# Kernel optimization log

Measured on AMD Instinct MI355X. Metric: run time of the kernel, lower is better.

## Reference

```python
import jax, jax.numpy as jnp
import numpy as np


def setup_inputs() -> dict:
    key = jax.random.key(0)
    ks = jax.random.split(key, 7)
    B, S, D, F, E = 4, 2048, 1024, 4096, 8
    scale = 0.02
    return {
        "x": jax.random.normal(ks[0], (B, S, D), dtype=jnp.float32),
        "gate_w": jax.random.normal(ks[1], (D, E), dtype=jnp.float32) * scale,
        "gate_b": jnp.zeros((E,), dtype=jnp.float32),
        "w1": jax.random.normal(ks[2], (E, D, F), dtype=jnp.float32) * scale,
        "b1": jnp.zeros((E, F), dtype=jnp.float32),
        "w2": jax.random.normal(ks[3], (E, F, D), dtype=jnp.float32) * scale,
        "b2": jnp.zeros((E, D), dtype=jnp.float32),
        "top_k": 2,
    }


def reference(x, gate_w, gate_b, w1, b1, w2, b2, top_k):
    B, S, D = x.shape
    E = w1.shape[0]
    xf = x.reshape(-1, D)                      # [T, D], T = B*S
    T = xf.shape[0]

    # Router: top-k logits, softmax over the selected k (as in torch code)
    logits = xf @ gate_w + gate_b              # [T, E]
    rw, sel = jax.lax.top_k(logits, top_k)     # [T, k], [T, k]
    w = jax.nn.softmax(rw, axis=-1)            # [T, k]

    # Dense combine weights: combine[t, e] = sum_k w[t,k] * (sel[t,k]==e)
    combine = jnp.zeros((T, E), dtype=xf.dtype)
    combine = combine.at[jnp.arange(T)[:, None], sel].add(w)

    # Loop over small fixed expert count; each expert FFN on all tokens,
    # weighted by combine (zero for unrouted tokens). Dropout p honored as 0 (eval).
    out = jnp.zeros_like(xf)
    for e in range(E):
        h = jax.nn.gelu(xf @ w1[e] + b1[e], approximate=False)  # torch F.gelu = exact
        out = out + combine[:, e:e + 1] * (h @ w2[e] + b2[e])
    return out.reshape(B, S, D)
```

## Files before the change

kernel.cpp:

```cpp
#include <hip/hip_runtime.h>
#include <math.h>

#define T_TOK 8192
#define DDIM  1024
#define FDIM  4096
#define NEXP  8
#define MAXT  136
#define NSLOT (2 * T_TOK)

typedef __attribute__((ext_vector_type(8))) short short8;
typedef __attribute__((ext_vector_type(4))) float f32x4;
typedef unsigned short u16;
typedef unsigned int   u32;

typedef const __attribute__((address_space(1))) u32* gp_t;
typedef       __attribute__((address_space(3))) u32* lp_t;

__device__ __forceinline__ void gload16(const void* g, void* l) {
  __builtin_amdgcn_global_load_lds((gp_t)g, (lp_t)l, 16, 0, 0);
}

#define VM6 asm volatile("s_waitcnt vmcnt(6)" ::: "memory")
#define VM0 asm volatile("s_waitcnt vmcnt(0)" ::: "memory")
#define SBAR __builtin_amdgcn_s_barrier()
#define SCHED0 __builtin_amdgcn_sched_barrier(0)

__device__ __forceinline__ u16 f2bf(float f) {
  u32 u = __float_as_uint(f);
  u = u + 0x7FFFu + ((u >> 16) & 1u);
  return (u16)(u >> 16);
}

__device__ __forceinline__ int imin(int a, int b) { return a < b ? a : b; }

__device__ __forceinline__ float gelu_fast(float v) {
  float u = 0.7978845608f * (v + 0.044715f * v * v * v);
  float t2 = __expf(2.f * u);
  float th = 1.f - 2.f / (t2 + 1.f);
  return 0.5f * v * (1.f + th);
}

__device__ __forceinline__ int xcd_swz(int orig, int nwg) {
  int xcd = orig & 7;
  int q = nwg >> 3, r = nwg & 7;
  int base = (xcd < r) ? xcd * (q + 1) : r * (q + 1) + (xcd - r) * q;
  return base + (orig >> 3);
}

__global__ __launch_bounds__(256) void router_kernel(
    const float* __restrict__ x, const float* __restrict__ gw,
    const float* __restrict__ gb, u16* __restrict__ xb,
    int* __restrict__ counts, int* __restrict__ sel, float* __restrict__ wts)
{
  const int t    = blockIdx.x * 4 + (threadIdx.x >> 6);
  const int lane = threadIdx.x & 63;
  const float* xr = x + (size_t)t * DDIM;
  u16* xbr = xb + (size_t)t * DDIM;
  float lg[NEXP];
  #pragma unroll
  for (int e = 0; e < NEXP; e++) lg[e] = 0.f;
  #pragma unroll
  for (int i = 0; i < 4; i++) {
    int d0 = i * 256 + lane * 4;
    float4 v = *(const float4*)(xr + d0);
    ushort4 o;
    o.x = f2bf(v.x); o.y = f2bf(v.y); o.z = f2bf(v.z); o.w = f2bf(v.w);
    *(ushort4*)(xbr + d0) = o;
    const float* g = gw + (size_t)d0 * NEXP;
    #pragma unroll
    for (int e = 0; e < NEXP; e++)
      lg[e] += v.x * g[e] + v.y * g[NEXP + e] + v.z * g[2 * NEXP + e] + v.w * g[3 * NEXP + e];
  }
  #pragma unroll
  for (int off = 32; off > 0; off >>= 1) {
    #pragma unroll
    for (int e = 0; e < NEXP; e++) lg[e] += __shfl_down(lg[e], off);
  }
  if (lane == 0) {
    float v0 = -1e30f, v1 = -1e30f; int s0 = 0, s1 = 0;
    #pragma unroll
    for (int e = 0; e < NEXP; e++) {
      float v = lg[e] + gb[e];
      if (v > v0) { v1 = v0; s1 = s0; v0 = v; s0 = e; }
      else if (v > v1) { v1 = v; s1 = e; }
    }
    float a  = expf(v1 - v0);
    float w0 = 1.f / (1.f + a);
    sel[t * 2] = s0; sel[t * 2 + 1] = s1;
    wts[t * 2] = w0; wts[t * 2 + 1] = 1.f - w0;
    atomicAdd(&counts[s0], 1); atomicAdd(&counts[s1], 1);
  }
}

__global__ __launch_bounds__(256) void scan_assign_kernel(
    const int* __restrict__ counts, const int* __restrict__ sel,
    const float* __restrict__ wts,
    int* __restrict__ offsets, int* __restrict__ map_e, int* __restrict__ map_r,
    int* __restrict__ nT, int* __restrict__ stok, float* __restrict__ swgt)
{
  __shared__ int spos[NEXP];
  if (threadIdx.x == 0) {
    int run = 0, nt = 0;
    for (int e = 0; e < NEXP; e++) {
      offsets[e] = run; spos[e] = run;
      int c = counts[e];
      int ntile = (c + 127) >> 7;
      for (int i = 0; i < ntile; i++) { map_e[nt] = e; map_r[nt] = i * 128; nt++; }
      run += c;
    }
    nT[0] = nt;
  }
  __syncthreads();
  for (int t = threadIdx.x; t < T_TOK; t += 256) {
    #pragma unroll
    for (int k = 0; k < 2; k++) {
      int e = sel[t * 2 + k];
      int p = atomicAdd(&spos[e], 1);
      stok[p] = t; swgt[p] = wts[t * 2 + k];
    }
  }
}

__global__ __launch_bounds__(256) void xgather_kernel(
    const u16* __restrict__ xb, const int* __restrict__ stok,
    u16* __restrict__ Xg)
{
  const int s = blockIdx.x * 2 + (threadIdx.x >> 7);
  const int u = threadIdx.x & 127;
  int tok = stok[s]; if ((u32)tok >= T_TOK) tok = 0;
  const uint4* src = (const uint4*)(xb + (size_t)tok * DDIM);
  uint4* dst = (uint4*)(Xg + (size_t)s * DDIM);
  dst[u] = src[u];
}

__global__ __launch_bounds__(256) void wtrans_kernel(
    const float* __restrict__ in, u16* __restrict__ out, int M, int N)
{
  const int e = blockIdx.z;
  in  += (size_t)e * M * N;
  out += (size_t)e * M * N;
  const int r0 = blockIdx.y * 128;
  const int c0 = blockIdx.x * 64;
  __shared__ float tile[128][65];
  const int tid = threadIdx.x;
  const int lr = tid >> 4;
  const int lc = (tid & 15) * 4;
  #pragma unroll
  for (int p = 0; p < 8; p++) {
    int r = p * 16 + lr;
    float4 v = *(const float4*)(in + (size_t)(r0 + r) * N + (c0 + lc));
    tile[r][lc] = v.x; tile[r][lc + 1] = v.y; tile[r][lc + 2] = v.z; tile[r][lc + 3] = v.w;
  }
  __syncthreads();
  const int oc = tid >> 4;
  const int om = (tid & 15) * 8;
  #pragma unroll
  for (int p = 0; p < 4; p++) {
    int c = p * 16 + oc;
    short8 o;
    #pragma unroll
    for (int j = 0; j < 8; j++) o[j] = (short)f2bf(tile[om + j][c]);
    *(short8*)(out + (size_t)(c0 + c) * M + (r0 + om)) = o;
  }
}

__global__ __launch_bounds__(512, 2) void gemm1_kernel(
    const u16* __restrict__ Xg, const u16* __restrict__ W1T,
    const float* __restrict__ B1,
    const int* __restrict__ counts, const int* __restrict__ offsets,
    const int* __restrict__ map_e, const int* __restrict__ map_r,
    const int* __restrict__ nT, u16* __restrict__ H)
{
  __shared__ __align__(16) char lds[3 * 49152];
  const int gid   = xcd_swz(blockIdx.x, gridDim.x);
  const int n_idx = gid / MAXT;
  const int t_idx = gid - n_idx * MAXT;
  if (t_idx >= nT[0]) return;
  const int e    = map_e[t_idx];
  const int row0 = map_r[t_idx];
  const int cnt  = counts[e];
  const int off  = offsets[e];
  const int n0   = n_idx * 256;

  const int tid = threadIdx.x, wave = tid >> 6, lane = tid & 63;
  const int lr = lane & 15, lq = lane >> 4;
  const int wr = wave >> 2, wc = wave & 3;
  const int l3 = lane >> 3;
  const int usrc = (lane & 7) ^ l3;

  const char* gA[2]; const char* gB[4];
  #pragma unroll
  for (int i = 0; i < 2; i++) {
    int rA = imin(off + row0 + wave * 16 + i * 8 + l3, NSLOT - 1);
    gA[i] = (const char*)Xg + (size_t)rA * 2048 + usrc * 16;
  }
  #pragma unroll
  for (int i = 0; i < 4; i++) {
    int rB = e * FDIM + n0 + wave * 32 + i * 8 + l3;
    gB[i] = (const char*)W1T + (size_t)rB * 2048 + usrc * 16;
  }

  auto stage = [&](int slot, int kByte) {
    char* base = lds + slot * 49152;
    #pragma unroll
    for (int i = 0; i < 2; i++)
      gload16(gA[i] + kByte, base + wave * 2048 + i * 1024 + lane * 16);
    #pragma unroll
    for (int i = 0; i < 4; i++)
      gload16(gB[i] + kByte, base + 16384 + wave * 4096 + i * 1024 + lane * 16);
  };

  f32x4 acc[4][4] = {};
  auto compute = [&](int slot) {
    const u16* A  = (const u16*)(lds + slot * 49152);
    const u16* Bp = (const u16*)(lds + slot * 49152 + 16384);
    #pragma unroll
    for (int ks = 0; ks < 2; ks++) {
      const int uu = ((ks * 4 + lq) ^ (lr & 7)) * 8;
      short8 a[4], b[4];
      #pragma unroll
      for (int n = 0; n < 4; n++)
        b[n] = *(const short8*)&Bp[(wc * 64 + n * 16 + lr) * 64 + uu];
      #pragma unroll
      for (int m = 0; m < 4; m++)
        a[m] = *(const short8*)&A[(wr * 64 + m * 16 + lr) * 64 + uu];
      #pragma unroll
      for (int m = 0; m < 4; m++)
        #pragma unroll
        for (int n = 0; n < 4; n++)
          acc[m][n] = __builtin_amdgcn_mfma_f32_16x16x32_bf16(a[m], b[n], acc[m][n], 0, 0, 0);
    }
  };

  stage(0, 0); stage(1, 128);
  VM6; SCHED0; SBAR; SCHED0;
  #pragma unroll 1
  for (int t = 0; t < 16; t++) {
    if (t + 2 < 16) stage((t + 2) % 3, (t + 2) * 128);
    compute(t % 3);
    SCHED0;
    if (t + 2 < 16)       { VM6; }
    else if (t + 2 == 16) { VM0; }
    SCHED0; SBAR; SCHED0;
  }

  #pragma unroll
  for (int m = 0; m < 4; m++) {
    int rloc = wr * 64 + m * 16 + lq * 4;
    #pragma unroll
    for (int j = 0; j < 4; j++) {
      int r = rloc + j;
      if (row0 + r < cnt) {
        u16* Hrow = H + (size_t)(off + row0 + r) * FDIM;
        #pragma unroll
        for (int n = 0; n < 4; n++) {
          int col = n0 + wc * 64 + n * 16 + lr;
          float v = acc[m][n][j] + B1[e * FDIM + col];
          Hrow[col] = f2bf(gelu_fast(v));
        }
      }
    }
  }
}

__global__ __launch_bounds__(512, 2) void gemm2_kernel(
    const u16* __restrict__ H, const u16* __restrict__ W2T,
    const float* __restrict__ B2,
    const int* __restrict__ counts, const int* __restrict__ offsets,
    const int* __restrict__ slot_token, const float* __restrict__ slot_weight,
    const int* __restrict__ map_e, const int* __restrict__ map_r,
    const int* __restrict__ nT, float* __restrict__ out)
{
  __shared__ __align__(16) char lds[3 * 49152];
  const int gid   = xcd_swz(blockIdx.x, gridDim.x);
  const int sp    = gid / (4 * MAXT);
  const int rem   = gid - sp * 4 * MAXT;
  const int n_idx = rem / MAXT;
  const int t_idx = rem - n_idx * MAXT;
  if (t_idx >= nT[0]) return;
  const int e    = map_e[t_idx];
  const int row0 = map_r[t_idx];
  const int cnt  = counts[e];
  const int off  = offsets[e];
  const int n0   = n_idx * 256;
  const int kbase = sp * 4096;

  const int tid = threadIdx.x, wave = tid >> 6, lane = tid & 63;
  const int lr = lane & 15, lq = lane >> 4;
  const int wr = wave >> 2, wc = wave & 3;
  const int l3 = lane >> 3;
  const int usrc = (lane & 7) ^ l3;

  const char* gA[2]; const char* gB[4];
  #pragma unroll
  for (int i = 0; i < 2; i++) {
    int rA = imin(off + row0 + wave * 16 + i * 8 + l3, NSLOT - 1);
    gA[i] = (const char*)H + (size_t)rA * 8192 + kbase + usrc * 16;
  }
  #pragma unroll
  for (int i = 0; i < 4; i++) {
    int rB = e * DDIM + n0 + wave * 32 + i * 8 + l3;
    gB[i] = (const char*)W2T + (size_t)rB * 8192 + kbase + usrc * 16;
  }

  auto stage = [&](int slot, int kByte) {
    char* base = lds + slot * 49152;
    #pragma unroll
    for (int i = 0; i < 2; i++)
      gload16(gA[i] + kByte, base + wave * 2048 + i * 1024 + lane * 16);
    #pragma unroll
    for (int i = 0; i < 4; i++)
      gload16(gB[i] + kByte, base + 16384 + wave * 4096 + i * 1024 + lane * 16);
  };

  f32x4 acc[4][4] = {};
  auto compute = [&](int slot) {
    const u16* A  = (const u16*)(lds + slot * 49152);
    const u16* Bp = (const u16*)(lds + slot * 49152 + 16384);
    #pragma unroll
    for (int ks = 0; ks < 2; ks++) {
      const int uu = ((ks * 4 + lq) ^ (lr & 7)) * 8;
      short8 a[4], b[4];
      #pragma unroll
      for (int n = 0; n < 4; n++)
        b[n] = *(const short8*)&Bp[(wc * 64 + n * 16 + lr) * 64 + uu];
      #pragma unroll
      for (int m = 0; m < 4; m++)
        a[m] = *(const short8*)&A[(wr * 64 + m * 16 + lr) * 64 + uu];
      #pragma unroll
      for (int m = 0; m < 4; m++)
        #pragma unroll
        for (int n = 0; n < 4; n++)
          acc[m][n] = __builtin_amdgcn_mfma_f32_16x16x32_bf16(a[m], b[n], acc[m][n], 0, 0, 0);
    }
  };

  stage(0, 0); stage(1, 128);
  VM6; SCHED0; SBAR; SCHED0;
  #pragma unroll 1
  for (int t = 0; t < 32; t++) {
    if (t + 2 < 32) stage((t + 2) % 3, (t + 2) * 128);
    compute(t % 3);
    SCHED0;
    if (t + 2 < 32)       { VM6; }
    else if (t + 2 == 32) { VM0; }
    SCHED0; SBAR; SCHED0;
  }

  #pragma unroll
  for (int m = 0; m < 4; m++) {
    int rloc = wr * 64 + m * 16 + lq * 4;
    #pragma unroll
    for (int j = 0; j < 4; j++) {
      int r = rloc + j;
      if (row0 + r >= cnt) continue;
      int s = off + row0 + r;
      int tok = slot_token[s];
      float wgt = slot_weight[s];
      #pragma unroll
      for (int n = 0; n < 4; n++) {
        int col = n0 + wc * 64 + n * 16 + lr;
        float v = acc[m][n][j];
        if (sp == 0) v += B2[e * DDIM + col];
        atomicAdd(&out[(size_t)tok * DDIM + col], wgt * v);
      }
    }
  }
}

extern "C" void kernel_launch(void* const* d_in, const int* in_sizes, int n_in,
                              void* d_out, int out_size, void* d_ws, size_t ws_size,
                              hipStream_t stream)
{
  (void)in_sizes; (void)n_in; (void)ws_size;
  const float* x  = (const float*)d_in[0];
  const float* gw = (const float*)d_in[1];
  const float* gb = (const float*)d_in[2];
  const float* w1 = (const float*)d_in[3];
  const float* b1 = (const float*)d_in[4];
  const float* w2 = (const float*)d_in[5];
  const float* b2 = (const float*)d_in[6];

  char* ws = (char*)d_ws;
  int*   counts = (int*)(ws + 0);
  int*   offp   = (int*)(ws + 64);
  int*   nT     = (int*)(ws + 128);
  int*   map_e  = (int*)(ws + 256);
  int*   map_r  = (int*)(ws + 1024);

  size_t p = 2048;
  int*   sel   = (int*)(ws + p);   p += (size_t)T_TOK * 2 * 4;
  float* wts   = (float*)(ws + p); p += (size_t)T_TOK * 2 * 4;
  int*   stok  = (int*)(ws + p);   p += (size_t)NSLOT * 4;
  float* swgt  = (float*)(ws + p); p += (size_t)NSLOT * 4;
  p = (p + 1048575) & ~(size_t)1048575;
  u16*   xb    = (u16*)(ws + p);   p += (size_t)T_TOK * DDIM * 2;
  u16*   Xg    = (u16*)(ws + p);   p += (size_t)NSLOT * DDIM * 2;
  u16*   w1t   = (u16*)(ws + p);   p += (size_t)NEXP * DDIM * FDIM * 2;
  u16*   w2t   = (u16*)(ws + p);   p += (size_t)NEXP * DDIM * FDIM * 2;
  u16*   Hbuf  = (u16*)(ws + p);

  hipMemsetAsync(ws, 0, 256, stream);
  hipMemsetAsync(d_out, 0, (size_t)out_size * sizeof(float), stream);
  router_kernel<<<T_TOK / 4, 256, 0, stream>>>(x, gw, gb, xb, counts, sel, wts);
  scan_assign_kernel<<<1, 256, 0, stream>>>(counts, sel, wts, offp, map_e, map_r, nT, stok, swgt);
  xgather_kernel<<<NSLOT / 2, 256, 0, stream>>>(xb, stok, Xg);
  wtrans_kernel<<<dim3(DDIM / 64, FDIM / 128, NEXP), 256, 0, stream>>>(w2, w2t, FDIM, DDIM);
  wtrans_kernel<<<dim3(FDIM / 64, DDIM / 128, NEXP), 256, 0, stream>>>(w1, w1t, DDIM, FDIM);

  gemm1_kernel<<<(FDIM / 256) * MAXT, 512, 0, stream>>>(
      Xg, w1t, b1, counts, offp, map_e, map_r, nT, Hbuf);
  gemm2_kernel<<<2 * (DDIM / 256) * MAXT, 512, 0, stream>>>(
      Hbuf, w2t, b2, counts, offp, stok, swgt, map_e, map_r, nT, (float*)d_out);
}
```

Baseline: 846.0 us.

## Fuse gather/convert and weight transposes into prep and GEMM kernels with smaller tiles

```diff
diff --git a/kernel.cpp b/kernel.cpp
--- a/kernel.cpp
+++ b/kernel.cpp
@@ -7,6 +7,8 @@
 #define NEXP  8
 #define MAXT  136
 #define NSLOT (2 * T_TOK)
+#define NG1   (32 * MAXT)
+#define NG2   (2 * 8 * MAXT)
 
 typedef __attribute__((ext_vector_type(8))) short short8;
 typedef __attribute__((ext_vector_type(4))) float f32x4;
@@ -19,11 +21,6 @@
 __device__ __forceinline__ void gload16(const void* g, void* l) {
   __builtin_amdgcn_global_load_lds((gp_t)g, (lp_t)l, 16, 0, 0);
 }
-
-#define VM6 asm volatile("s_waitcnt vmcnt(6)" ::: "memory")
-#define VM0 asm volatile("s_waitcnt vmcnt(0)" ::: "memory")
-#define SBAR __builtin_amdgcn_s_barrier()
-#define SCHED0 __builtin_amdgcn_sched_barrier(0)
 
 __device__ __forceinline__ u16 f2bf(float f) {
   u32 u = __float_as_uint(f);
@@ -49,13 +46,12 @@
 
 __global__ __launch_bounds__(256) void router_kernel(
     const float* __restrict__ x, const float* __restrict__ gw,
-    const float* __restrict__ gb, u16* __restrict__ xb,
+    const float* __restrict__ gb,
     int* __restrict__ counts, int* __restrict__ sel, float* __restrict__ wts)
 {
   const int t    = blockIdx.x * 4 + (threadIdx.x >> 6);
   const int lane = threadIdx.x & 63;
   const float* xr = x + (size_t)t * DDIM;
-  u16* xbr = xb + (size_t)t * DDIM;
   float lg[NEXP];
   #pragma unroll
   for (int e = 0; e < NEXP; e++) lg[e] = 0.f;
@@ -63,9 +59,6 @@
   for (int i = 0; i < 4; i++) {
     int d0 = i * 256 + lane * 4;
     float4 v = *(const float4*)(xr + d0);
-    ushort4 o;
-    o.x = f2bf(v.x); o.y = f2bf(v.y); o.z = f2bf(v.z); o.w = f2bf(v.w);
-    *(ushort4*)(xbr + d0) = o;
     const float* g = gw + (size_t)d0 * NEXP;
     #pragma unroll
     for (int e = 0; e < NEXP; e++)
@@ -121,58 +114,83 @@
   }
 }
 
-__global__ __launch_bounds__(256) void xgather_kernel(
-    const u16* __restrict__ xb, const int* __restrict__ stok,
-    u16* __restrict__ Xg)
-{
-  const int s = blockIdx.x * 2 + (threadIdx.x >> 7);
-  const int u = threadIdx.x & 127;
+__device__ void wtrans_tile(float* __restrict__ tile,
+                            const float* __restrict__ in, u16* __restrict__ out,
+                            int M, int N, int r0, int c0)
+{
+  const int tid = threadIdx.x;
+  const int tr = tid >> 4, tc = (tid & 15) * 4;
+  #pragma unroll
+  for (int p = 0; p < 4; p++) {
+    int r = p * 16 + tr;
+    float4 v = *(const float4*)(in + (size_t)(r0 + r) * N + (c0 + tc));
+    tile[r * 65 + tc]     = v.x; tile[r * 65 + tc + 1] = v.y;
+    tile[r * 65 + tc + 2] = v.z; tile[r * 65 + tc + 3] = v.w;
+  }
+  __syncthreads();
+  const int oc = tid >> 3, om = (tid & 7) * 8;
+  #pragma unroll
+  for (int p = 0; p < 2; p++) {
+    int c = p * 32 + oc;
+    short8 o;
+    #pragma unroll
+    for (int j = 0; j < 8; j++) o[j] = (short)f2bf(tile[(om + j) * 65 + c]);
+    *(short8*)(out + (size_t)(c0 + c) * M + (r0 + om)) = o;
+  }
+  __syncthreads();
+}
+
+__global__ __launch_bounds__(256) void prep1_kernel(
+    const float* __restrict__ x, const int* __restrict__ stok,
+    u16* __restrict__ Xg, const float* __restrict__ w1, u16* __restrict__ w1t)
+{
+  __shared__ __align__(16) float tile[64 * 65];
+  const int b = blockIdx.x;
+  if (b % 17 == 16) {
+    int w = b / 17;
+    #pragma unroll 1
+    for (int i = 0; i < 8; i++) {
+      int t = w * 8 + i;
+      int e = t >> 10, rem = t & 1023;
+      int tn = rem >> 4, tm = rem & 15;
+      wtrans_tile(tile, w1 + (size_t)e * DDIM * FDIM,
+                  w1t + (size_t)e * DDIM * FDIM, DDIM, FDIM, tm * 64, tn * 64);
+    }
+    return;
+  }
+  int s = b - b / 17;
   int tok = stok[s]; if ((u32)tok >= T_TOK) tok = 0;
-  const uint4* src = (const uint4*)(xb + (size_t)tok * DDIM);
-  uint4* dst = (uint4*)(Xg + (size_t)s * DDIM);
-  dst[u] = src[u];
-}
-
-__global__ __launch_bounds__(256) void wtrans_kernel(
-    const float* __restrict__ in, u16* __restrict__ out, int M, int N)
-{
-  const int e = blockIdx.z;
-  in  += (size_t)e * M * N;
-  out += (size_t)e * M * N;
-  const int r0 = blockIdx.y * 128;
-  const int c0 = blockIdx.x * 64;
-  __shared__ float tile[128][65];
-  const int tid = threadIdx.x;
-  const int lr = tid >> 4;
-  const int lc = (tid & 15) * 4;
-  #pragma unroll
-  for (int p = 0; p < 8; p++) {
-    int r = p * 16 + lr;
-    float4 v = *(const float4*)(in + (size_t)(r0 + r) * N + (c0 + lc));
-    tile[r][lc] = v.x; tile[r][lc + 1] = v.y; tile[r][lc + 2] = v.z; tile[r][lc + 3] = v.w;
-  }
-  __syncthreads();
-  const int oc = tid >> 4;
-  const int om = (tid & 15) * 8;
-  #pragma unroll
-  for (int p = 0; p < 4; p++) {
-    int c = p * 16 + oc;
-    short8 o;
-    #pragma unroll
-    for (int j = 0; j < 8; j++) o[j] = (short)f2bf(tile[om + j][c]);
-    *(short8*)(out + (size_t)(c0 + c) * M + (r0 + om)) = o;
-  }
-}
-
-__global__ __launch_bounds__(512, 2) void gemm1_kernel(
+  float4 v = *(const float4*)(x + (size_t)tok * DDIM + threadIdx.x * 4);
+  ushort4 o;
+  o.x = f2bf(v.x); o.y = f2bf(v.y); o.z = f2bf(v.z); o.w = f2bf(v.w);
+  *(ushort4*)(Xg + (size_t)s * DDIM + threadIdx.x * 4) = o;
+}
+
+__global__ __launch_bounds__(256) void gemm1_kernel(
     const u16* __restrict__ Xg, const u16* __restrict__ W1T,
     const float* __restrict__ B1,
     const int* __restrict__ counts, const int* __restrict__ offsets,
     const int* __restrict__ map_e, const int* __restrict__ map_r,
-    const int* __restrict__ nT, u16* __restrict__ H)
-{
-  __shared__ __align__(16) char lds[3 * 49152];
-  const int gid   = xcd_swz(blockIdx.x, gridDim.x);
+    const int* __restrict__ nT, u16* __restrict__ H,
+    const float* __restrict__ w2, u16* __restrict__ w2t)
+{
+  __shared__ __align__(16) char lds[64 * 65 * 4];
+  const int b = blockIdx.x;
+  if (b < 4608 && (b % 9) == 8) {
+    int w = b / 9;
+    float* tile = (float*)lds;
+    #pragma unroll 1
+    for (int i = 0; i < 16; i++) {
+      int t = w * 16 + i;
+      int e = t >> 10, rem = t & 1023;
+      int tm = rem >> 4, tn = rem & 15;
+      wtrans_tile(tile, w2 + (size_t)e * FDIM * DDIM,
+                  w2t + (size_t)e * FDIM * DDIM, FDIM, DDIM, tm * 64, tn * 64);
+    }
+    return;
+  }
+  const int gemmIdx = (b < 4608) ? (b - b / 9) : (b - 512);
+  const int gid   = xcd_swz(gemmIdx, NG1);
   const int n_idx = gid / MAXT;
   const int t_idx = gid - n_idx * MAXT;
   if (t_idx >= nT[0]) return;
@@ -180,90 +198,67 @@
   const int row0 = map_r[t_idx];
   const int cnt  = counts[e];
   const int off  = offsets[e];
-  const int n0   = n_idx * 256;
-
+  const int n0   = n_idx * 128;
+
+  u16* As = (u16*)lds;
+  u16* Bs = (u16*)(lds + 8192);
   const int tid = threadIdx.x, wave = tid >> 6, lane = tid & 63;
   const int lr = lane & 15, lq = lane >> 4;
-  const int wr = wave >> 2, wc = wave & 3;
-  const int l3 = lane >> 3;
-  const int usrc = (lane & 7) ^ l3;
-
-  const char* gA[2]; const char* gB[4];
+  const int wr = wave >> 1, wc = wave & 1;
+  const int l2 = lane >> 2, lb = (lane & 3) * 16;
+
+  const char* gA[2]; const char* gB[2];
   #pragma unroll
   for (int i = 0; i < 2; i++) {
-    int rA = imin(off + row0 + wave * 16 + i * 8 + l3, NSLOT - 1);
-    gA[i] = (const char*)Xg + (size_t)rA * 2048 + usrc * 16;
-  }
-  #pragma unroll
-  for (int i = 0; i < 4; i++) {
-    int rB = e * FDIM + n0 + wave * 32 + i * 8 + l3;
-    gB[i] = (const char*)W1T + (size_t)rB * 2048 + usrc * 16;
-  }
-
-  auto stage = [&](int slot, int kByte) {
-    char* base = lds + slot * 49152;
-    #pragma unroll
-    for (int i = 0; i < 2; i++)
-      gload16(gA[i] + kByte, base + wave * 2048 + i * 1024 + lane * 16);
-    #pragma unroll
-    for (int i = 0; i < 4; i++)
-      gload16(gB[i] + kByte, base + 16384 + wave * 4096 + i * 1024 + lane * 16);
-  };
+    int R = (wave * 2 + i) * 16 + l2;
+    int aidx = imin(off + row0 + R, NSLOT - 1);
+    gA[i] = (const char*)Xg + (size_t)aidx * 2048 + lb;
+    gB[i] = (const char*)W1T + (size_t)(e * FDIM + n0 + R) * 2048 + lb;
+  }
 
   f32x4 acc[4][4] = {};
-  auto compute = [&](int slot) {
-    const u16* A  = (const u16*)(lds + slot * 49152);
-    const u16* Bp = (const u16*)(lds + slot * 49152 + 16384);
-    #pragma unroll
-    for (int ks = 0; ks < 2; ks++) {
-      const int uu = ((ks * 4 + lq) ^ (lr & 7)) * 8;
-      short8 a[4], b[4];
+  #pragma unroll 1
+  for (int k0 = 0; k0 < 2048; k0 += 64) {
+    __syncthreads();
+    gload16(gA[0] + k0, lds + (wave * 2) * 1024 + lane * 16);
+    gload16(gA[1] + k0, lds + (wave * 2 + 1) * 1024 + lane * 16);
+    gload16(gB[0] + k0, lds + 8192 + (wave * 2) * 1024 + lane * 16);
+    gload16(gB[1] + k0, lds + 8192 + (wave * 2 + 1) * 1024 + lane * 16);
+    __syncthreads();
+    short8 a[4], bf[4];
+    #pragma unroll
+    for (int m = 0; m < 4; m++)
+      a[m] = *(const short8*)&As[(wr * 64 + m * 16 + lr) * 32 + lq * 8];
+    #pragma unroll
+    for (int n = 0; n < 4; n++)
+      bf[n] = *(const short8*)&Bs[(wc * 64 + n * 16 + lr) * 32 + lq * 8];
+    #pragma unroll
+    for (int m = 0; m < 4; m++)
       #pragma unroll
       for (int n = 0; n < 4; n++)
-        b[n] = *(const short8*)&Bp[(wc * 64 + n * 16 + lr) * 64 + uu];
+        acc[m][n] = __builtin_amdgcn_mfma_f32_16x16x32_bf16(a[m], bf[n], acc[m][n], 0, 0, 0);
+  }
+
+  #pragma unroll
+  for (int nn = 0; nn < 4; nn++) {
+    int col = n0 + wc * 64 + nn * 16 + lr;
+    float b1v = B1[e * FDIM + col];
+    #pragma unroll
+    for (int m = 0; m < 4; m++) {
+      int rbase = wr * 64 + m * 16 + lq * 4;
       #pragma unroll
-      for (int m = 0; m < 4; m++)
-        a[m] = *(const short8*)&A[(wr * 64 + m * 16 + lr) * 64 + uu];
-      #pragma unroll
-      for (int m = 0; m < 4; m++)
-        #pragma unroll
-        for (int n = 0; n < 4; n++)
-          acc[m][n] = __builtin_amdgcn_mfma_f32_16x16x32_bf16(a[m], b[n], acc[m][n], 0, 0, 0);
-    }
-  };
-
-  stage(0, 0); stage(1, 128);
-  VM6; SCHED0; SBAR; SCHED0;
-  #pragma unroll 1
-  for (int t = 0; t < 16; t++) {
-    if (t + 2 < 16) stage((t + 2) % 3, (t + 2) * 128);
-    compute(t % 3);
-    SCHED0;
-    if (t + 2 < 16)       { VM6; }
-    else if (t + 2 == 16) { VM0; }
-    SCHED0; SBAR; SCHED0;
-  }
-
-  #pragma unroll
-  for (int m = 0; m < 4; m++) {
-    int rloc = wr * 64 + m * 16 + lq * 4;
-    #pragma unroll
-    for (int j = 0; j < 4; j++) {
-      int r = rloc + j;
-      if (row0 + r < cnt) {
-        u16* Hrow = H + (size_t)(off + row0 + r) * FDIM;
-        #pragma unroll
-        for (int n = 0; n < 4; n++) {
-          int col = n0 + wc * 64 + n * 16 + lr;
-          float v = acc[m][n][j] + B1[e * FDIM + col];
-          Hrow[col] = f2bf(gelu_fast(v));
+      for (int j = 0; j < 4; j++) {
+        int r = rbase + j;
+        if (row0 + r < cnt) {
+          float v = acc[m][nn][j] + b1v;
+          H[(size_t)(off + row0 + r) * FDIM + col] = f2bf(gelu_fast(v));
         }
       }
     }
   }
 }
 
-__global__ __launch_bounds__(512, 2) void gemm2_kernel(
+__global__ __launch_bounds__(256) void gemm2_kernel(
     const u16* __restrict__ H, const u16* __restrict__ W2T,
     const float* __restrict__ B2,
     const int* __restrict__ counts, const int* __restrict__ offsets,
@@ -271,10 +266,10 @@
     const int* __restrict__ map_e, const int* __restrict__ map_r,
     const int* __restrict__ nT, float* __restrict__ out)
 {
-  __shared__ __align__(16) char lds[3 * 49152];
-  const int gid   = xcd_swz(blockIdx.x, gridDim.x);
-  const int sp    = gid / (4 * MAXT);
-  const int rem   = gid - sp * 4 * MAXT;
+  __shared__ __align__(16) char lds[16384];
+  const int gid   = xcd_swz(blockIdx.x, NG2);
+  const int sp    = gid / (8 * MAXT);
+  const int rem   = gid - sp * 8 * MAXT;
   const int n_idx = rem / MAXT;
   const int t_idx = rem - n_idx * MAXT;
   if (t_idx >= nT[0]) return;
@@ -282,77 +277,54 @@
   const int row0 = map_r[t_idx];
   const int cnt  = counts[e];
   const int off  = offsets[e];
-  const int n0   = n_idx * 256;
+  const int n0   = n_idx * 128;
   const int kbase = sp * 4096;
 
+  u16* As = (u16*)lds;
+  u16* Bs = (u16*)(lds + 8192);
   const int tid = threadIdx.x, wave = tid >> 6, lane = tid & 63;
   const int lr = lane & 15, lq = lane >> 4;
-  const int wr = wave >> 2, wc = wave & 3;
-  const int l3 = lane >> 3;
-  const int usrc = (lane & 7) ^ l3;
-
-  const char* gA[2]; const char* gB[4];
+  const int wr = wave >> 1, wc = wave & 1;
+  const int l2 = lane >> 2, lb = (lane & 3) * 16;
+
+  const char* gA[2]; const char* gB[2];
   #pragma unroll
   for (int i = 0; i < 2; i++) {
-    int rA = imin(off + row0 + wave * 16 + i * 8 + l3, NSLOT - 1);
-    gA[i] = (const char*)H + (size_t)rA * 8192 + kbase + usrc * 16;
-  }
-  #pragma unroll
-  for (int i = 0; i < 4; i++) {
-    int rB = e * DDIM + n0 + wave * 32 + i * 8 + l3;
-    gB[i] = (const char*)W2T + (size_t)rB * 8192 + kbase + usrc * 16;
-  }
-
-  auto stage = [&](int slot, int kByte) {
-    char* base = lds + slot * 49152;
-    #pragma unroll
-    for (int i = 0; i < 2; i++)
-      gload16(gA[i] + kByte, base + wave * 2048 + i * 1024 + lane * 16);
-    #pragma unroll
-    for (int i = 0; i < 4; i++)
-      gload16(gB[i] + kByte, base + 16384 + wave * 4096 + i * 1024 + lane * 16);
-  };
+    int R = (wave * 2 + i) * 16 + l2;
+    int aidx = imin(off + row0 + R, NSLOT - 1);
+    gA[i] = (const char*)H + (size_t)aidx * 8192 + kbase + lb;
+    gB[i] = (const char*)W2T + (size_t)(e * DDIM + n0 + R) * 8192 + kbase + lb;
+  }
 
   f32x4 acc[4][4] = {};
-  auto compute = [&](int slot) {
-    const u16* A  = (const u16*)(lds + slot * 49152);
-    const u16* Bp = (const u16*)(lds + slot * 49152 + 16384);
-    #pragma unroll
-    for (int ks = 0; ks < 2; ks++) {
-      const int uu = ((ks * 4 + lq) ^ (lr & 7)) * 8;
-      short8 a[4], b[4];
+  #pragma unroll 1
+  for (int k0 = 0; k0 < 4096; k0 += 64) {
+    __syncthreads();
+    gload16(gA[0] + k0, lds + (wave * 2) * 1024 + lane * 16);
+    gload16(gA[1] + k0, lds + (wave * 2 + 1) * 1024 + lane * 16);
+    gload16(gB[0] + k0, lds + 8192 + (wave * 2) * 1024 + lane * 16);
+    gload16(gB[1] + k0, lds + 8192 + (wave * 2 + 1) * 1024 + lane * 16);
+    __syncthreads();
+    short8 a[4], bf[4];
+    #pragma unroll
+    for (int m = 0; m < 4; m++)
+      a[m] = *(const short8*)&As[(wr * 64 + m * 16 + lr) * 32 + lq * 8];
+    #pragma unroll
+    for (int n = 0; n < 4; n++)
+      bf[n] = *(const short8*)&Bs[(wc * 64 + n * 16 + lr) * 32 + lq * 8];
+    #pragma unroll
+    for (int m = 0; m < 4; m++)
       #pragma unroll
       for (int n = 0; n < 4; n++)
-        b[n] = *(const short8*)&Bp[(wc * 64 + n * 16 + lr) * 64 + uu];
-      #pragma unroll
-      for (int m = 0; m < 4; m++)
-        a[m] = *(const short8*)&A[(wr * 64 + m * 16 + lr) * 64 + uu];
-      #pragma unroll
-      for (int m = 0; m < 4; m++)
-        #pragma unroll
-        for (int n = 0; n < 4; n++)
-          acc[m][n] = __builtin_amdgcn_mfma_f32_16x16x32_bf16(a[m], b[n], acc[m][n], 0, 0, 0);
-    }
-  };
-
-  stage(0, 0); stage(1, 128);
-  VM6; SCHED0; SBAR; SCHED0;
-  #pragma unroll 1
-  for (int t = 0; t < 32; t++) {
-    if (t + 2 < 32) stage((t + 2) % 3, (t + 2) * 128);
-    compute(t % 3);
-    SCHED0;
-    if (t + 2 < 32)       { VM6; }
-    else if (t + 2 == 32) { VM0; }
-    SCHED0; SBAR; SCHED0;
+        acc[m][n] = __builtin_amdgcn_mfma_f32_16x16x32_bf16(a[m], bf[n], acc[m][n], 0, 0, 0);
   }
 
   #pragma unroll
   for (int m = 0; m < 4; m++) {
-    int rloc = wr * 64 + m * 16 + lq * 4;
+    int rbase = wr * 64 + m * 16 + lq * 4;
     #pragma unroll
     for (int j = 0; j < 4; j++) {
-      int r = rloc + j;
+      int r = rbase + j;
       if (row0 + r >= cnt) continue;
       int s = off + row0 + r;
       int tok = slot_token[s];
@@ -394,7 +366,6 @@
   int*   stok  = (int*)(ws + p);   p += (size_t)NSLOT * 4;
   float* swgt  = (float*)(ws + p); p += (size_t)NSLOT * 4;
   p = (p + 1048575) & ~(size_t)1048575;
-  u16*   xb    = (u16*)(ws + p);   p += (size_t)T_TOK * DDIM * 2;
   u16*   Xg    = (u16*)(ws + p);   p += (size_t)NSLOT * DDIM * 2;
   u16*   w1t   = (u16*)(ws + p);   p += (size_t)NEXP * DDIM * FDIM * 2;
   u16*   w2t   = (u16*)(ws + p);   p += (size_t)NEXP * DDIM * FDIM * 2;
@@ -402,14 +373,11 @@
 
   hipMemsetAsync(ws, 0, 256, stream);
   hipMemsetAsync(d_out, 0, (size_t)out_size * sizeof(float), stream);
-  router_kernel<<<T_TOK / 4, 256, 0, stream>>>(x, gw, gb, xb, counts, sel, wts);
+  router_kernel<<<T_TOK / 4, 256, 0, stream>>>(x, gw, gb, counts, sel, wts);
   scan_assign_kernel<<<1, 256, 0, stream>>>(counts, sel, wts, offp, map_e, map_r, nT, stok, swgt);
-  xgather_kernel<<<NSLOT / 2, 256, 0, stream>>>(xb, stok, Xg);
-  wtrans_kernel<<<dim3(DDIM / 64, FDIM / 128, NEXP), 256, 0, stream>>>(w2, w2t, FDIM, DDIM);
-  wtrans_kernel<<<dim3(FDIM / 64, DDIM / 128, NEXP), 256, 0, stream>>>(w1, w1t, DDIM, FDIM);
-
-  gemm1_kernel<<<(FDIM / 256) * MAXT, 512, 0, stream>>>(
-      Xg, w1t, b1, counts, offp, map_e, map_r, nT, Hbuf);
-  gemm2_kernel<<<2 * (DDIM / 256) * MAXT, 512, 0, stream>>>(
+  prep1_kernel<<<NSLOT + 1024, 256, 0, stream>>>(x, stok, Xg, w1, w1t);
+  gemm1_kernel<<<NG1 + 512, 256, 0, stream>>>(
+      Xg, w1t, b1, counts, offp, map_e, map_r, nT, Hbuf, w2, w2t);
+  gemm2_kernel<<<NG2, 256, 0, stream>>>(
       Hbuf, w2t, b2, counts, offp, stok, swgt, map_e, map_r, nT, (float*)d_out);
 }
```

Result: slower. 962.3 us (+13.8%).
